# Optimization experiments

Hardware: AMD Instinct MI355X
Metric: run time of the kernel (lower is better)

Reference implementation:

```python
import jax, jax.numpy as jnp
import numpy as np

N_WIRES = 4
DIM = 16  # 2**N_WIRES

# PauliZ eigenvalue signs per wire per basis state (wire 0 = MSB, torchquantum convention)
_Z = np.array([[1.0 - 2.0 * ((i >> (N_WIRES - 1 - w)) & 1) for i in range(DIM)]
               for w in range(N_WIRES)], dtype=np.float32)  # [4,16]

def _cnot_perm(c, t):
    mc = 1 << (N_WIRES - 1 - c)
    mt = 1 << (N_WIRES - 1 - t)
    return np.array([i ^ mt if (i & mc) else i for i in range(DIM)])

_PERM_WRAP = [_cnot_perm(0, 1), _cnot_perm(1, 2), _cnot_perm(2, 3), _cnot_perm(3, 0)]  # QLSTM ladder
_PERM_LINE = [_cnot_perm(0, 1), _cnot_perm(1, 2), _cnot_perm(2, 3)]                   # kernel ladder

def _apply_rx(state, theta, wire):
    """Apply RX(theta) on `wire`. state: [B,16] complex64. theta: scalar or [B]."""
    theta = jnp.asarray(theta)
    c = jnp.cos(theta / 2).astype(jnp.complex64)
    s = jnp.sin(theta / 2).astype(jnp.complex64)
    left = 2 ** wire
    right = 2 ** (N_WIRES - 1 - wire)
    st = state.reshape(-1, left, 2, right)
    a, b = st[:, :, 0, :], st[:, :, 1, :]
    if theta.ndim != 0:
        c = c[:, None, None]
        s = s[:, None, None]
    na = c * a - 1j * s * b
    nb = -1j * s * a + c * b
    return jnp.stack([na, nb], axis=2).reshape(-1, DIM)

def _circuit(angles, params, perms):
    """angles: [B,4] encoding RX angles; params: [4] trainable RX angles."""
    B = angles.shape[0]
    state = jnp.zeros((B, DIM), jnp.complex64).at[:, 0].set(1.0)
    for w in range(N_WIRES):
        state = _apply_rx(state, angles[:, w], w)
    for w in range(N_WIRES):
        state = _apply_rx(state, params[w], w)
    for p in perms:
        state = state[:, p]
    return state

def _measure_z(state):
    probs = state.real ** 2 + state.imag ** 2  # [B,16]
    return probs @ jnp.asarray(_Z).T           # [B,4]

def setup_inputs() -> dict:
    key = jax.random.key(0)
    ks = jax.random.split(key, 16)
    T, B, D, S, H = 128, 64, 32, 1024, 4
    inp = {
        'x': jax.random.normal(ks[0], (T, B, D), jnp.float32),
        'support_vectors': jax.random.normal(ks[1], (S, D), jnp.float32),
        'Wf': jax.random.normal(ks[2], (H, D + H), jnp.float32) * 0.1,
        'bf': jax.random.normal(ks[3], (H,), jnp.float32) * 0.1,
        'Wi': jax.random.normal(ks[4], (H, D + H), jnp.float32) * 0.1,
        'bi': jax.random.normal(ks[5], (H,), jnp.float32) * 0.1,
        'Wu': jax.random.normal(ks[6], (H, D + H), jnp.float32) * 0.1,
        'bu': jax.random.normal(ks[7], (H,), jnp.float32) * 0.1,
        'Wo': jax.random.normal(ks[8], (H, D + H), jnp.float32) * 0.1,
        'bo': jax.random.normal(ks[9], (H,), jnp.float32) * 0.1,
        'pf': jax.random.normal(ks[10], (H,), jnp.float32),
        'pi': jax.random.normal(ks[11], (H,), jnp.float32),
        'pu': jax.random.normal(ks[12], (H,), jnp.float32),
        'po': jax.random.normal(ks[13], (H,), jnp.float32),
        'qk_params': jax.random.normal(ks[14], (H,), jnp.float32),
    }
    return inp

def reference(x, support_vectors, Wf, bf, Wi, bi, Wu, bu, Wo, bo, pf, pi, pu, po, qk_params):
    T, B, D = x.shape
    gamma = 1.0
    xf = x.reshape(T * B, D)

    # classical RBF Gram matrix (materializes [N,S,D] diff, as in the original)
    diff = xf[:, None, :] - support_vectors[None, :, :]
    rbf = jnp.exp(-gamma * jnp.sum(diff * diff, axis=-1))  # [N,S]

    # quantum kernel: encode first 4 features, trainable RX, linear CNOT ladder
    sx = _circuit(xf[:, :4], qk_params, _PERM_LINE)               # [N,16] complex
    sy = _circuit(support_vectors[:, :4], qk_params, _PERM_LINE)  # [S,16] complex
    qk = jnp.abs(sx @ sy.T)  # no conjugation, matching torch.matmul(states_x, states_y.t())

    def gate(comb, W, b, p):
        return _measure_z(_circuit(comb @ W.T + b, p, _PERM_WRAP))

    def step(carry, xt):
        hx, cx = carry
        comb = jnp.concatenate([xt, hx], axis=1)
        f = jax.nn.sigmoid(gate(comb, Wf, bf, pf))
        i = jax.nn.sigmoid(gate(comb, Wi, bi, pi))
        g = jnp.tanh(gate(comb, Wu, bu, pu))
        o = jax.nn.sigmoid(gate(comb, Wo, bo, po))
        cx = f * cx + i * g
        hx = o * jnp.tanh(cx)
        return (hx, cx), hx

    h0 = jnp.zeros((B, N_WIRES), jnp.float32)
    c0 = jnp.zeros((B, N_WIRES), jnp.float32)
    (_, _), outs = jax.lax.scan(step, (h0, c0), x)  # outs: [T,B,4]
    return (outs, rbf, qk)
```

## Files before the change

kernel.cpp:

```cpp
#include <hip/hip_runtime.h>

#define T_STEPS 128
#define BATCH   64
#define DIMX    32
#define S_SUP   1024
#define NROW    8192
#define OUT_H_SZ   (T_STEPS*BATCH*4)
#define OUT_RBF_SZ (NROW*S_SUP)

#define INV2PI 0.15915494309189535f
#define L2E    1.4426950408889634f

__device__ __forceinline__ float rcp_fast(float x)  { return __builtin_amdgcn_rcpf(x); }
__device__ __forceinline__ float exp2_fast(float x) { return __builtin_amdgcn_exp2f(x); }
__device__ __forceinline__ float cos_rev(float x)   { return __builtin_amdgcn_cosf(x); }

template<int CTRL>
__device__ __forceinline__ float dpp_perm(float v) {
    return __builtin_bit_cast(float,
        __builtin_amdgcn_mov_dpp(__builtin_bit_cast(int, v), CTRL, 0xF, 0xF, true));
}
template<int K>
__device__ __forceinline__ float quad_bcast(float v) { return dpp_perm<K * 0x55>(v); }
#define DPP_SHL8 0x108
#define DPP_SHR8 0x118

__device__ __forceinline__ float xor8(float v) {
    return dpp_perm<DPP_SHL8>(v) + dpp_perm<DPP_SHR8>(v);
}

__global__ __launch_bounds__(256) void pre_kernel(
    const float* __restrict__ x,
    const float* __restrict__ Wf, const float* __restrict__ bf,
    const float* __restrict__ Wi, const float* __restrict__ bi,
    const float* __restrict__ Wu, const float* __restrict__ bu,
    const float* __restrict__ Wo, const float* __restrict__ bo,
    const float* __restrict__ pf, const float* __restrict__ pi,
    const float* __restrict__ pu, const float* __restrict__ po,
    float* __restrict__ pre)
{
    const int tid = threadIdx.x;
    const int rl  = tid >> 4;
    const int gw  = tid & 15;
    const int g   = gw >> 2, w = gw & 3;
    const int row = blockIdx.x * 16 + rl;

    __shared__ float xs[16 * DIMX];
    if (tid < 128) {
        ((float4*)xs)[tid] = ((const float4*)(x + (size_t)blockIdx.x * 16 * DIMX))[tid];
    }
    __syncthreads();

    const float* W  = (g == 0) ? Wf : (g == 1) ? Wi : (g == 2) ? Wu : Wo;
    const float* bb = (g == 0) ? bf : (g == 1) ? bi : (g == 2) ? bu : bo;
    const float* pp = (g == 0) ? pf : (g == 1) ? pi : (g == 2) ? pu : po;

    float acc = bb[w] + pp[w];
    const float* Wr = W + w * 36;
    const float* xr = xs + rl * DIMX;
#pragma unroll
    for (int d = 0; d < DIMX; d++) acc += xr[d] * Wr[d];

    pre[(row * 4 + g) * 4 + w] = acc * INV2PI;
}

__global__ __launch_bounds__(512, 2) void fused_kernel(
    const float* __restrict__ x,  const float* __restrict__ sv,
    const float* __restrict__ Wf, const float* __restrict__ bf,
    const float* __restrict__ Wi, const float* __restrict__ bi,
    const float* __restrict__ Wu, const float* __restrict__ bu,
    const float* __restrict__ Wo, const float* __restrict__ bo,
    const float* __restrict__ pf, const float* __restrict__ pi,
    const float* __restrict__ pu, const float* __restrict__ po,
    const float* __restrict__ qkp, const float* __restrict__ pre,
    float* __restrict__ out_h, float* __restrict__ out_rbf, float* __restrict__ out_qk)
{
    __shared__ float xs[32 * DIMX];
    __shared__ float xn2[32];
    const int tid = threadIdx.x;

    if (blockIdx.x == 0) {
        __builtin_amdgcn_s_setprio(3);
        const int lane = tid & 63;
        const int wv   = tid >> 6;
        const int g    = lane & 3;
        const int wp   = (lane >> 3) & 1;
        const int bl   = ((lane >> 4) << 1) | ((lane >> 2) & 1);
        const int b    = wv * 8 + bl;
        const bool iswp = wp != 0;
        const bool selB = ((lane >> 1) & 1) != 0;
        const int wown  = 2 * wp + ((lane >> 1) & 1);
        const int hbase = b * 4 + wown;

        const float* W = (g == 0) ? Wf : (g == 1) ? Wi : (g == 2) ? Wu : Wo;
        const int wA = 2 * wp;
        const int p0 = 2 * wp, p1 = 2 * wp + 1, p2 = 2 - 2 * wp, p3 = 3 - 2 * wp;
        float WhA[4], WhB[4];
        WhA[0] = W[ wA      * 36 + 32 + p0] * INV2PI;
        WhA[1] = W[ wA      * 36 + 32 + p1] * INV2PI;
        WhA[2] = W[ wA      * 36 + 32 + p2] * INV2PI;
        WhA[3] = W[ wA      * 36 + 32 + p3] * INV2PI;
        WhB[0] = W[(wA + 1) * 36 + 32 + p0] * INV2PI;
        WhB[1] = W[(wA + 1) * 36 + 32 + p1] * INV2PI;
        WhB[2] = W[(wA + 1) * 36 + 32 + p2] * INV2PI;
        WhB[3] = W[(wA + 1) * 36 + 32 + p3] * INV2PI;

        const float K2 = (g == 2) ? (-2.f * L2E) : (-L2E);
        const float Aa = (g == 2) ? (-4.f * L2E) : 1.f;
        const float Bb = (g == 2) ? ( 2.f * L2E) : 0.f;

        float h = 0.f, cs = 0.f;
        const float2* prep2 = (const float2*)pre;
        const int pbase = b * 8 + g * 2 + wp;

        auto lstm_step = [&](int t, float2 cur) {
            float hXa = quad_bcast<0>(h);
            float hXb = quad_bcast<2>(h);
            float hYa = xor8(hXa);
            float hYb = xor8(hXb);

            float aA = cur.x + hXa * WhA[0] + hXb * WhA[1] + hYa * WhA[2] + hYb * WhA[3];
            float aB = cur.y + hXa * WhB[0] + hXb * WhB[1] + hYa * WhB[2] + hYb * WhB[3];
            float CA = cos_rev(aA), CB = cos_rev(aB);

            float DA = xor8(CA);
            float DB = xor8(CB);

            float P  = DA * DB;
            float t1 = iswp ? CA : CB;
            float rA = t1 * P;
            float t2 = iswp ? rA : CA;
            float rB = t2 * CB;

            float sA = rcp_fast(1.f + exp2_fast(rA * K2));
            float sB = rcp_fast(1.f + exp2_fast(rB * K2));
            float oA = fmaf(Aa, sA, Bb);
            float oB = fmaf(Aa, sB, Bb);

            float Fa = quad_bcast<0>(oA), Fb = quad_bcast<0>(oB);
            float Ia = quad_bcast<1>(oA), Ib = quad_bcast<1>(oB);
            float Ua = quad_bcast<2>(oA), Ub = quad_bcast<2>(oB);
            float Oa = quad_bcast<3>(oA), Ob = quad_bcast<3>(oB);
            float F = selB ? Fb : Fa;
            float I = selB ? Ib : Ia;
            float U = selB ? Ub : Ua;
            float O = selB ? Ob : Oa;

            cs = fmaf(F, cs, I * U);
            float th = fmaf(2.f, rcp_fast(1.f + exp2_fast(cs)), -1.f);
            h = O * th;

            out_h[t * 256 + hbase] = h;
        };

        float2 cb0, cb1, cb2, cb3, cb4, cb5, cb6, cb7;
        cb0 = prep2[pbase];            cb1 = prep2[pbase + 512];
        cb2 = prep2[pbase + 1024];     cb3 = prep2[pbase + 1536];
        cb4 = prep2[pbase + 2048];     cb5 = prep2[pbase + 2560];
        cb6 = prep2[pbase + 3072];     cb7 = prep2[pbase + 3584];

#pragma unroll 1
        for (int tt = 0; tt < T_STEPS; tt += 8) {
            int nb = tt + 8; nb = (nb > T_STEPS - 8) ? (T_STEPS - 8) : nb;
            const float2* pc = prep2 + pbase + nb * 512;
            float2 nb0 = pc[0];
            float2 nb1 = pc[512];
            float2 nb2 = pc[1024];
            float2 nb3 = pc[1536];
            float2 nb4 = pc[2048];
            float2 nb5 = pc[2560];
            float2 nb6 = pc[3072];
            float2 nb7 = pc[3584];
            __builtin_amdgcn_sched_barrier(0);

            lstm_step(tt + 0, cb0);
            lstm_step(tt + 1, cb1);
            lstm_step(tt + 2, cb2);
            lstm_step(tt + 3, cb3);
            lstm_step(tt + 4, cb4);
            lstm_step(tt + 5, cb5);
            lstm_step(tt + 6, cb6);
            lstm_step(tt + 7, cb7);

            cb0 = nb0; cb1 = nb1; cb2 = nb2; cb3 = nb3;
            cb4 = nb4; cb5 = nb5; cb6 = nb6; cb7 = nb7;
        }
    } else {
        const int bid = blockIdx.x - 1;
        const int n0  = bid * 32;

        float4* xs4 = (float4*)xs;
        const float4* xg = (const float4*)(x + (size_t)n0 * DIMX);
        if (tid < 256) {
            float4 t0v = xg[tid];
            xs4[tid] = t0v;
            float p0 = t0v.x * t0v.x + t0v.y * t0v.y + t0v.z * t0v.z + t0v.w * t0v.w;
            p0 += __shfl_xor(p0, 1);
            p0 += __shfl_xor(p0, 2);
            p0 += __shfl_xor(p0, 4);
            if ((tid & 7) == 0) xn2[tid >> 3] = -L2E * p0;
        }

        const int sA = tid, sB = tid + 512;
        float4 svv[8], svw[8];
        const float4* svgA = (const float4*)(sv + (size_t)sA * DIMX);
        const float4* svgB = (const float4*)(sv + (size_t)sB * DIMX);
#pragma unroll
        for (int k = 0; k < 8; k++) { svv[k] = svgA[k]; svw[k] = svgB[k]; }
        float sn2A = 0.f, sn2B = 0.f;
#pragma unroll
        for (int k = 0; k < 8; k++) {
            sn2A += svv[k].x * svv[k].x + svv[k].y * svv[k].y + svv[k].z * svv[k].z + svv[k].w * svv[k].w;
            sn2B += svw[k].x * svw[k].x + svw[k].y * svw[k].y + svw[k].z * svw[k].z + svw[k].w * svw[k].w;
        }
        const float snlA = -L2E * sn2A;
        const float snlB = -L2E * sn2B;

        const float q0 = qkp[0], q1 = qkp[1], q2 = qkp[2], q3 = qkp[3];
        const float C05 = 0.5f * INV2PI;
        const float BA0 = fmaf(0.5f, svv[0].x, q0) * INV2PI;
        const float BA1 = fmaf(0.5f, svv[0].y, q1) * INV2PI;
        const float BA2 = fmaf(0.5f, svv[0].z, q2) * INV2PI;
        const float BA3 = fmaf(0.5f, svv[0].w, q3) * INV2PI;
        const float BB0 = fmaf(0.5f, svw[0].x, q0) * INV2PI;
        const float BB1 = fmaf(0.5f, svw[0].y, q1) * INV2PI;
        const float BB2 = fmaf(0.5f, svw[0].z, q2) * INV2PI;
        const float BB3 = fmaf(0.5f, svw[0].w, q3) * INV2PI;
        __syncthreads();

#pragma unroll 2
        for (int n = 0; n < 32; n++) {
            const float4* xr4 = (const float4*)(xs + n * DIMX);
            float4 xv0 = xr4[0];
            float dotA = xv0.x * svv[0].x + xv0.y * svv[0].y + xv0.z * svv[0].z + xv0.w * svv[0].w;
            float dotB = xv0.x * svw[0].x + xv0.y * svw[0].y + xv0.z * svw[0].z + xv0.w * svw[0].w;
#pragma unroll
            for (int k = 1; k < 8; k++) {
                float4 xv = xr4[k];
                dotA += xv.x * svv[k].x + xv.y * svv[k].y + xv.z * svv[k].z + xv.w * svv[k].w;
                dotB += xv.x * svw[k].x + xv.y * svw[k].y + xv.z * svw[k].z + xv.w * svw[k].w;
            }
            float xnl = xn2[n];
            float rbA = exp2_fast(fmaf(2.f * L2E, dotA, xnl + snlA));
            float rbB = exp2_fast(fmaf(2.f * L2E, dotB, xnl + snlB));

            float qvA = cos_rev(fmaf(C05, xv0.x, BA0)) * cos_rev(fmaf(C05, xv0.y, BA1))
                      * cos_rev(fmaf(C05, xv0.z, BA2)) * cos_rev(fmaf(C05, xv0.w, BA3));
            float qvB = cos_rev(fmaf(C05, xv0.x, BB0)) * cos_rev(fmaf(C05, xv0.y, BB1))
                      * cos_rev(fmaf(C05, xv0.z, BB2)) * cos_rev(fmaf(C05, xv0.w, BB3));
            qvA = fabsf(qvA);
            qvB = fabsf(qvB);

            const size_t rowb = (size_t)(n0 + n) * S_SUP;
            out_rbf[rowb + sA] = rbA;
            out_rbf[rowb + sB] = rbB;
            out_qk [rowb + sA] = qvA;
            out_qk [rowb + sB] = qvB;
        }
    }
}

extern "C" void kernel_launch(void* const* d_in, const int* in_sizes, int n_in,
                              void* d_out, int out_size, void* d_ws, size_t ws_size,
                              hipStream_t stream)
{
    const float* x   = (const float*)d_in[0];
    const float* sv  = (const float*)d_in[1];
    const float* Wf  = (const float*)d_in[2];
    const float* bf  = (const float*)d_in[3];
    const float* Wi  = (const float*)d_in[4];
    const float* bi  = (const float*)d_in[5];
    const float* Wu  = (const float*)d_in[6];
    const float* bu  = (const float*)d_in[7];
    const float* Wo  = (const float*)d_in[8];
    const float* bo  = (const float*)d_in[9];
    const float* pf  = (const float*)d_in[10];
    const float* pi  = (const float*)d_in[11];
    const float* pu  = (const float*)d_in[12];
    const float* po  = (const float*)d_in[13];
    const float* qkp = (const float*)d_in[14];

    float* out     = (float*)d_out;
    float* out_h   = out;
    float* out_rbf = out + OUT_H_SZ;
    float* out_qk  = out + OUT_H_SZ + OUT_RBF_SZ;

    float* pre = (float*)d_ws;

    pre_kernel<<<NROW / 16, 256, 0, stream>>>(x, Wf, bf, Wi, bi, Wu, bu, Wo, bo,
                                              pf, pi, pu, po, pre);
    fused_kernel<<<1 + 256, 512, 0, stream>>>(
        x, sv, Wf, bf, Wi, bi, Wu, bu, Wo, bo, pf, pi, pu, po, qkp, pre,
        out_h, out_rbf, out_qk);
}
```

Before: 142.1 us.

## Split LSTM recurrence over two blocks and use polynomial gate activations

New measurement: 133.2 us. -6.3%, faster.

```diff
diff --git a/kernel.cpp b/kernel.cpp
--- a/kernel.cpp
+++ b/kernel.cpp
@@ -79,14 +79,15 @@
     __shared__ float xn2[32];
     const int tid = threadIdx.x;
 
-    if (blockIdx.x == 0) {
+    if (blockIdx.x < 2) {
+        if (tid >= 256) return;
         __builtin_amdgcn_s_setprio(3);
         const int lane = tid & 63;
         const int wv   = tid >> 6;
         const int g    = lane & 3;
         const int wp   = (lane >> 3) & 1;
         const int bl   = ((lane >> 4) << 1) | ((lane >> 2) & 1);
-        const int b    = wv * 8 + bl;
+        const int b    = blockIdx.x * 32 + wv * 8 + bl;
         const bool iswp = wp != 0;
         const bool selB = ((lane >> 1) & 1) != 0;
         const int wown  = 2 * wp + ((lane >> 1) & 1);
@@ -105,11 +106,12 @@
         WhB[2] = W[(wA + 1) * 36 + 32 + p2] * INV2PI;
         WhB[3] = W[(wA + 1) * 36 + 32 + p3] * INV2PI;
 
-        const float K2 = (g == 2) ? (-2.f * L2E) : (-L2E);
-        const float Aa = (g == 2) ? (-4.f * L2E) : 1.f;
-        const float Bb = (g == 2) ? ( 2.f * L2E) : 0.f;
-
-        float h = 0.f, cs = 0.f;
+        const float S1 = 0.25f;
+        const float S3 = -2.0833334e-2f;
+        const float S5 =  2.0833334e-3f;
+        const float S7 = -2.1081349e-4f;
+
+        float h = 0.f, c = 0.f;
         const float2* prep2 = (const float2*)pre;
         const int pbase = b * 8 + g * 2 + wp;
 
@@ -119,8 +121,12 @@
             float hYa = xor8(hXa);
             float hYb = xor8(hXb);
 
-            float aA = cur.x + hXa * WhA[0] + hXb * WhA[1] + hYa * WhA[2] + hYb * WhA[3];
-            float aB = cur.y + hXa * WhB[0] + hXb * WhB[1] + hYa * WhB[2] + hYb * WhB[3];
+            float eA = fmaf(hXb, WhA[1], fmaf(hXa, WhA[0], cur.x));
+            float fA = fmaf(hYb, WhA[3], hYa * WhA[2]);
+            float aA = eA + fA;
+            float eB = fmaf(hXb, WhB[1], fmaf(hXa, WhB[0], cur.y));
+            float fB = fmaf(hYb, WhB[3], hYa * WhB[2]);
+            float aB = eB + fB;
             float CA = cos_rev(aA), CB = cos_rev(aB);
 
             float DA = xor8(CA);
@@ -132,23 +138,32 @@
             float t2 = iswp ? rA : CA;
             float rB = t2 * CB;
 
-            float sA = rcp_fast(1.f + exp2_fast(rA * K2));
-            float sB = rcp_fast(1.f + exp2_fast(rB * K2));
-            float oA = fmaf(Aa, sA, Bb);
-            float oB = fmaf(Aa, sB, Bb);
-
-            float Fa = quad_bcast<0>(oA), Fb = quad_bcast<0>(oB);
-            float Ia = quad_bcast<1>(oA), Ib = quad_bcast<1>(oB);
-            float Ua = quad_bcast<2>(oA), Ub = quad_bcast<2>(oB);
-            float Oa = quad_bcast<3>(oA), Ob = quad_bcast<3>(oB);
+            float qA = rA * rA, qB = rB * rB;
+            float pA  = fmaf(qA, fmaf(qA, fmaf(qA, S7, S5), S3), S1);
+            float pB  = fmaf(qB, fmaf(qB, fmaf(qB, S7, S5), S3), S1);
+            float sgA = fmaf(rA, pA, 0.5f);
+            float sgB = fmaf(rB, pB, 0.5f);
+            float nA  = rA * fmaf(qA, qA + 105.f, 945.f);
+            float dA  = fmaf(qA, fmaf(qA, 15.f, 420.f), 945.f);
+            float thA = nA * rcp_fast(dA);
+            float nB  = rB * fmaf(qB, qB + 105.f, 945.f);
+            float dB  = fmaf(qB, fmaf(qB, 15.f, 420.f), 945.f);
+            float thB = nB * rcp_fast(dB);
+
+            float Fa = quad_bcast<0>(sgA), Fb = quad_bcast<0>(sgB);
+            float Ia = quad_bcast<1>(sgA), Ib = quad_bcast<1>(sgB);
+            float Ua = quad_bcast<2>(thA), Ub = quad_bcast<2>(thB);
+            float Oa = quad_bcast<3>(sgA), Ob = quad_bcast<3>(sgB);
             float F = selB ? Fb : Fa;
             float I = selB ? Ib : Ia;
             float U = selB ? Ub : Ua;
             float O = selB ? Ob : Oa;
 
-            cs = fmaf(F, cs, I * U);
-            float th = fmaf(2.f, rcp_fast(1.f + exp2_fast(cs)), -1.f);
-            h = O * th;
+            c = fmaf(F, c, I * U);
+            float qc = c * c;
+            float nc = c * fmaf(qc, qc + 105.f, 945.f);
+            float dc = fmaf(qc, fmaf(qc, 15.f, 420.f), 945.f);
+            h = O * (nc * rcp_fast(dc));
 
             out_h[t * 256 + hbase] = h;
         };
@@ -186,7 +201,7 @@
             cb4 = nb4; cb5 = nb5; cb6 = nb6; cb7 = nb7;
         }
     } else {
-        const int bid = blockIdx.x - 1;
+        const int bid = blockIdx.x - 2;
         const int n0  = bid * 32;
 
         float4* xs4 = (float4*)xs;
@@ -289,7 +304,7 @@
 
     pre_kernel<<<NROW / 16, 256, 0, stream>>>(x, Wf, bf, Wi, bi, Wu, bu, Wo, bo,
                                               pf, pi, pu, po, pre);
-    fused_kernel<<<1 + 256, 512, 0, stream>>>(
+    fused_kernel<<<2 + 256, 512, 0, stream>>>(
         x, sv, Wf, bf, Wi, bi, Wu, bu, Wo, bo, pf, pi, pu, po, qkp, pre,
         out_h, out_rbf, out_qk);
 }
```
